# Kernel tuning notes

Measured on AMD Instinct MI355X. Metric: run time of the kernel, lower is better.

## Reference

```python
import jax, jax.numpy as jnp
import numpy as np

WINDOW_SIZE = 2
SOFTMAX_TEMP = 0.01


def get_indices(batch_size, window_size):
    # For each window, match keypoints of frame j against dense map of frame j+1.
    kp_inds, dense_inds = [], []
    for i in range(batch_size):
        for j in range(window_size - 1):
            idx = i * window_size + j
            kp_inds.append(idx)
            dense_inds.append(idx + 1)
    return np.array(kp_inds), np.array(dense_inds)


def l2_normalize(x, axis):
    n = jnp.sqrt(jnp.sum(x * x, axis=axis, keepdims=True))
    return x / jnp.maximum(n, 1e-12)


def grid_sample_bilinear(img, grid_u, grid_v):
    """torch.nn.functional.grid_sample, mode='bilinear', padding='zeros', align_corners=False.
    img: (B,C,H,W); grid_u, grid_v: (B,N) normalized coords in [-1,1]. Returns (B,C,N)."""
    B, C, H, W = img.shape
    x = ((grid_u + 1.0) * W - 1.0) * 0.5  # pixel x
    y = ((grid_v + 1.0) * H - 1.0) * 0.5  # pixel y
    x0 = jnp.floor(x)
    y0 = jnp.floor(y)
    wx1 = x - x0
    wy1 = y - y0
    flat = img.reshape(B, C, H * W)

    def gather(xi, yi):
        valid = (xi >= 0) & (xi <= W - 1) & (yi >= 0) & (yi <= H - 1)
        xi_c = jnp.clip(xi, 0, W - 1).astype(jnp.int32)
        yi_c = jnp.clip(yi, 0, H - 1).astype(jnp.int32)
        idx = yi_c * W + xi_c  # (B,N)
        vals = jnp.take_along_axis(flat, idx[:, None, :], axis=2)  # (B,C,N)
        return vals * valid[:, None, :].astype(img.dtype)

    out = (gather(x0, y0) * ((1 - wx1) * (1 - wy1))[:, None, :]
           + gather(x0 + 1, y0) * (wx1 * (1 - wy1))[:, None, :]
           + gather(x0, y0 + 1) * ((1 - wx1) * wy1)[:, None, :]
           + gather(x0 + 1, y0 + 1) * (wx1 * wy1)[:, None, :])
    return out


def setup_inputs() -> dict:
    key = jax.random.key(0)
    k1, k2, k3, k4 = jax.random.split(key, 4)
    BW, C, N, H, W = 8, 128, 512, 256, 256
    return {
        "keypoint_scores": jax.random.uniform(k1, (BW, 1, N), dtype=jnp.float32),
        "keypoint_desc": jax.random.normal(k2, (BW, C, N), dtype=jnp.float32),
        "scores_dense": jax.random.uniform(k3, (BW, 1, H, W), dtype=jnp.float32),
        "desc_dense": jax.random.normal(k4, (BW, C, H, W), dtype=jnp.float32),
    }


def reference(keypoint_scores, keypoint_desc, scores_dense, desc_dense):
    BW, C, N = keypoint_desc.shape
    batch_size = BW // WINDOW_SIZE
    _, _, H, W = desc_dense.shape
    kp_inds, dense_inds = get_indices(batch_size, WINDOW_SIZE)

    src_desc = l2_normalize(keypoint_desc[kp_inds], axis=1)  # (B,C,N)
    B = src_desc.shape[0]
    tgt_desc_dense = desc_dense[dense_inds]  # (B,C,H,W)
    tgt_unrolled = l2_normalize(tgt_desc_dense.reshape(B, C, H * W), axis=1)

    # cosine similarity scores (B,N,H*W) -> temperature softmax over dense map
    match_vals = jnp.einsum('bcn,bcm->bnm', src_desc, tgt_unrolled)
    soft_match_vals = jax.nn.softmax(match_vals / SOFTMAX_TEMP, axis=2)

    # soft-argmax: expected (u,v) pixel coordinates
    v_coord, u_coord = jnp.meshgrid(jnp.arange(H), jnp.arange(W), indexing='ij')
    coords = jnp.stack([u_coord.reshape(-1), v_coord.reshape(-1)], axis=1).astype(jnp.float32)  # (HW,2)
    pseudo_coords = jnp.einsum('bnm,mk->bnk', soft_match_vals, coords)  # (B,N,2)

    u_norm = 2.0 * pseudo_coords[:, :, 0] / (W - 1) - 1.0
    v_norm = 2.0 * pseudo_coords[:, :, 1] / (H - 1) - 1.0

    tgt_scores_dense = scores_dense[dense_inds]
    pseudo_scores = grid_sample_bilinear(tgt_scores_dense, u_norm, v_norm)  # (B,1,N)
    pseudo_desc = grid_sample_bilinear(tgt_desc_dense, u_norm, v_norm)      # (B,C,N)

    desc_match_score = jnp.sum(src_desc * pseudo_desc, axis=1, keepdims=True) / float(C)
    src_scores = keypoint_scores[kp_inds]
    match_weights = 0.5 * (desc_match_score + 1.0) * src_scores * pseudo_scores
    return (pseudo_coords, match_weights, soft_match_vals)
```

## Files before the change

kernel.cpp:

```cpp
#include <hip/hip_runtime.h>


typedef short  v8s __attribute__((ext_vector_type(8)));
typedef unsigned short v8u __attribute__((ext_vector_type(8)));
typedef float  v4f __attribute__((ext_vector_type(4)));

#define EXP2_SCALE 144.269504088896f
#define WAITV(N) asm volatile("s_waitcnt vmcnt(" #N ")" ::: "memory")
#define SBAR()   __builtin_amdgcn_s_barrier()
#define SCHED()  __builtin_amdgcn_sched_barrier(0)

static const size_t O_AHI  = 0;
static const size_t O_ALO  = O_AHI  + 262144ull*2;
static const size_t O_SRCN = O_ALO  + 262144ull*2;
static const size_t O_BHI  = O_SRCN + 262144ull*4;
static const size_t O_BLO  = O_BHI  + 33554432ull*2;
static const size_t O_PART = O_BLO  + 33554432ull*2;
static const size_t O_ROWS = O_PART + 2048ull*512*16;

static __device__ inline unsigned short f2bf(float x) {
    unsigned u = __float_as_uint(x);
    u = u + 0x7FFFu + ((u >> 16) & 1u);
    return (unsigned short)(u >> 16);
}
static __device__ inline float bf2f(unsigned short h) {
    return __uint_as_float(((unsigned)h) << 16);
}

__device__ __forceinline__ void gl_lds16(const void* g, void* l) {
    auto gp = (const __attribute__((address_space(1))) unsigned int*)(uintptr_t)g;
    auto lp = (__attribute__((address_space(3))) unsigned int*)(uintptr_t)l;
    __builtin_amdgcn_global_load_lds(gp, lp, 16, 0, 0);
}

__global__ void __launch_bounds__(256) k_prep_src(const float* __restrict__ kd,
                                                  float* __restrict__ srcN,
                                                  unsigned short* __restrict__ Ahi,
                                                  unsigned short* __restrict__ Alo) {
    int gw = blockIdx.x * 4 + (threadIdx.x >> 6);
    int l  = threadIdx.x & 63;
    int b  = gw >> 9, n = gw & 511;
    const float* base = kd + (size_t)(2 * b) * 128 * 512;
    float x0 = base[l * 512 + n];
    float x1 = base[(l + 64) * 512 + n];
    float ss = x0 * x0 + x1 * x1;
#pragma unroll
    for (int m = 1; m < 64; m <<= 1) ss += __shfl_xor(ss, m, 64);
    float inv = 1.0f / fmaxf(sqrtf(ss), 1e-12f);
    float xn0 = x0 * inv, xn1 = x1 * inv;
    int ob = gw * 128;
    srcN[ob + l] = xn0;  srcN[ob + l + 64] = xn1;
    unsigned short h0 = f2bf(xn0), h1 = f2bf(xn1);
    Ahi[ob + l] = h0;        Ahi[ob + l + 64] = h1;
    Alo[ob + l] = f2bf(xn0 - bf2f(h0));
    Alo[ob + l + 64] = f2bf(xn1 - bf2f(h1));
}

__global__ void __launch_bounds__(256) k_prep_tgt(const float* __restrict__ dd,
                                                  unsigned short* __restrict__ Bhi,
                                                  unsigned short* __restrict__ Blo) {
    int t = blockIdx.x * 128 + (threadIdx.x >> 1);
    int h = threadIdx.x & 1;
    int b = t >> 16;
    int p = t & 65535;
    const float* src = dd + (size_t)(2 * b + 1) * 128 * 65536 + (size_t)(h * 64) * 65536 + p;
    float v[64];
    float ss = 0.f;
#pragma unroll
    for (int c = 0; c < 64; ++c) { float x = src[(size_t)c * 65536]; v[c] = x; ss += x * x; }
    ss += __shfl_xor(ss, 1, 64);
    float inv = 1.0f / fmaxf(sqrtf(ss), 1e-12f);
    size_t ob = (size_t)t * 128 + h * 64;
#pragma unroll
    for (int c8 = 0; c8 < 8; ++c8) {
        v8u h8, l8;
#pragma unroll
        for (int j = 0; j < 8; ++j) {
            float xn = v[c8 * 8 + j] * inv;
            unsigned short hh = f2bf(xn);
            h8[j] = hh;
            l8[j] = f2bf(xn - bf2f(hh));
        }
        *(v8u*)(Bhi + ob + c8 * 8) = h8;
        *(v8u*)(Blo + ob + c8 * 8) = l8;
    }
}

template <int MODE>
__global__ void __launch_bounds__(512, 2) k_gemm(const unsigned short* __restrict__ Ahi,
                                                 const unsigned short* __restrict__ Alo,
                                                 const unsigned short* __restrict__ Bhi,
                                                 const unsigned short* __restrict__ Blo,
                                                 const float4* __restrict__ rows,
                                                 float* __restrict__ part,
                                                 float* __restrict__ out,
                                                 const float* __restrict__ ksc,
                                                 const float* __restrict__ sd,
                                                 const float* __restrict__ dd,
                                                 const float* __restrict__ srcN) {
    __shared__ v4f bstage4[4096];
    char* bstage = (char*)bstage4;

    const int tid = threadIdx.x;
    const int l = tid & 63, w = tid >> 6;
    const int wm = w >> 2, wn = w & 3;
    const int l15 = l & 15, l16 = l >> 4;
    const int mtg = blockIdx.x, ny = blockIdx.y, b = blockIdx.z;
    const int mt0 = mtg * 16;
    float* osm = out + 6144;

    v8s ahi[2][4], alo[2][4];
    {
        const size_t ar = ((size_t)(b * 512 + ny * 128 + wn * 32 + l15)) * 128 + l16 * 8;
#pragma unroll
        for (int nf = 0; nf < 2; ++nf)
#pragma unroll
            for (int ksl = 0; ksl < 4; ++ksl) {
                ahi[nf][ksl] = *(const v8s*)(Ahi + ar + nf * 2048 + ksl * 32);
                alo[nf][ksl] = *(const v8s*)(Alo + ar + nf * 2048 + ksl * 32);
            }
    }
    float invs[2];
    if (MODE == 1) {
#pragma unroll
        for (int nf = 0; nf < 2; ++nf)
            invs[nf] = rows[b * 512 + ny * 128 + wn * 32 + nf * 16 + l15].x;
    }
    WAITV(0);

    size_t pxrow = ((size_t)b * 65536 + (size_t)mt0 * 128) * 128;

#define STAGEU(SRC, prow, bufidx)                                                   \
    {                                                                               \
        const unsigned short* src_ = (SRC) + (prow);                                \
        char* dst_ = bstage + (bufidx) * 32768;                                     \
        _Pragma("unroll")                                                           \
        for (int i = 0; i < 4; ++i) {                                               \
            int sl = tid + i * 512;                                                 \
            int rl = sl >> 4, gg = sl & 15;                                         \
            gl_lds16(src_ + rl * 128 + ((gg ^ (rl & 15)) << 3), dst_ + (sl << 4));  \
        }                                                                           \
    }

#define PXF(bufbase, mf_, ksl_)                                                     \
    (*(const v8s*)((bufbase) + (wm * 64 + (mf_) * 16 + l15) * 256 +                 \
                   ((((ksl_) * 4 + l16) ^ ((wm * 64 + (mf_) * 16 + l15) & 15)) << 4)))

    v4f acc[4][2];

    if (MODE == 0) {
        STAGEU(Bhi, pxrow, 0);
        for (int mt = 0; mt < 16; ++mt) {
            if (mt < 15) STAGEU(Bhi, pxrow + 16384, (mt + 1) & 1);
            if (mt == 0) WAITV(4); else if (mt == 15) WAITV(0); else WAITV(6);
            SBAR(); SCHED();
            const char* bb = bstage + (mt & 1) * 32768;
#pragma unroll
            for (int mf = 0; mf < 4; ++mf)
#pragma unroll
                for (int nf = 0; nf < 2; ++nf) { v4f z = {0.f,0.f,0.f,0.f}; acc[mf][nf] = z; }
#pragma unroll
            for (int ksl = 0; ksl < 4; ++ksl) {
                v8s pxf[4];
#pragma unroll
                for (int mf = 0; mf < 4; ++mf) pxf[mf] = PXF(bb, mf, ksl);
#pragma unroll
                for (int mf = 0; mf < 4; ++mf)
#pragma unroll
                    for (int nf = 0; nf < 2; ++nf) {
                        acc[mf][nf] = __builtin_amdgcn_mfma_f32_16x16x32_bf16(pxf[mf], ahi[nf][ksl], acc[mf][nf], 0, 0, 0);
                        acc[mf][nf] = __builtin_amdgcn_mfma_f32_16x16x32_bf16(pxf[mf], alo[nf][ksl], acc[mf][nf], 0, 0, 0);
                    }
            }
            SCHED(); SBAR();
            float sS[2] = {0.f, 0.f}, sM[2] = {0.f, 0.f};
#pragma unroll
            for (int mf = 0; mf < 4; ++mf) {
                int mloc = wm * 64 + mf * 16 + l16 * 4;
#pragma unroll
                for (int nf = 0; nf < 2; ++nf)
#pragma unroll
                    for (int r = 0; r < 4; ++r) {
                        float e = __builtin_amdgcn_exp2f(fmaf(acc[mf][nf][r], EXP2_SCALE, -EXP2_SCALE));
                        sS[nf] += e;
                        sM[nf] = fmaf(e, (float)(mloc + r), sM[nf]);
                    }
            }
#pragma unroll
            for (int nf = 0; nf < 2; ++nf) {
                sS[nf] += __shfl_xor(sS[nf], 16, 64); sS[nf] += __shfl_xor(sS[nf], 32, 64);
                sM[nf] += __shfl_xor(sM[nf], 16, 64); sM[nf] += __shfl_xor(sM[nf], 32, 64);
            }
            if (l < 16) {
#pragma unroll
                for (int nf = 0; nf < 2; ++nf) {
                    int row = b * 512 + ny * 128 + wn * 32 + nf * 16 + l15;
                    *(float2*)(part + (((size_t)row * 512 + (mt0 + mt)) * 2 + wm) * 2)
                        = make_float2(sS[nf], sM[nf]);
                }
            }
            pxrow += 16384;
        }
    } else {
        STAGEU(Bhi, pxrow, 0);
        for (int mt = 0; mt < 16; ++mt) {
            STAGEU(Blo, pxrow, 1);
            if (mt == 0) WAITV(4); else WAITV(12);
            SBAR(); SCHED();
            const char* b0 = bstage;
#pragma unroll
            for (int mf = 0; mf < 4; ++mf)
#pragma unroll
                for (int nf = 0; nf < 2; ++nf) { v4f z = {0.f,0.f,0.f,0.f}; acc[mf][nf] = z; }
#pragma unroll
            for (int ksl = 0; ksl < 4; ++ksl) {
                v8s pxf[4];
#pragma unroll
                for (int mf = 0; mf < 4; ++mf) pxf[mf] = PXF(b0, mf, ksl);
#pragma unroll
                for (int mf = 0; mf < 4; ++mf)
#pragma unroll
                    for (int nf = 0; nf < 2; ++nf) {
                        acc[mf][nf] = __builtin_amdgcn_mfma_f32_16x16x32_bf16(pxf[mf], ahi[nf][ksl], acc[mf][nf], 0, 0, 0);
                        acc[mf][nf] = __builtin_amdgcn_mfma_f32_16x16x32_bf16(pxf[mf], alo[nf][ksl], acc[mf][nf], 0, 0, 0);
                    }
            }
            SCHED(); SBAR();
            if (mt < 15) STAGEU(Bhi, pxrow + 16384, 0);
            if (mt == 15) WAITV(0); else WAITV(4);
            SBAR(); SCHED();
            const char* b1 = bstage + 32768;
#pragma unroll
            for (int ksl = 0; ksl < 4; ++ksl) {
                v8s pxf[4];
#pragma unroll
                for (int mf = 0; mf < 4; ++mf) pxf[mf] = PXF(b1, mf, ksl);
#pragma unroll
                for (int mf = 0; mf < 4; ++mf)
#pragma unroll
                    for (int nf = 0; nf < 2; ++nf)
                        acc[mf][nf] = __builtin_amdgcn_mfma_f32_16x16x32_bf16(pxf[mf], ahi[nf][ksl], acc[mf][nf], 0, 0, 0);
            }
            SCHED(); SBAR();
            size_t mg0 = (size_t)(mt0 + mt) * 128 + wm * 64 + l16 * 4;
#pragma unroll
            for (int mf = 0; mf < 4; ++mf)
#pragma unroll
                for (int nf = 0; nf < 2; ++nf) {
                    v4f pv;
#pragma unroll
                    for (int r = 0; r < 4; ++r)
                        pv[r] = __builtin_amdgcn_exp2f(fmaf(acc[mf][nf][r], EXP2_SCALE, -EXP2_SCALE)) * invs[nf];
                    size_t ng = (size_t)(b * 512 + ny * 128 + wn * 32 + nf * 16 + l15);
                    __builtin_nontemporal_store(pv, (v4f*)(osm + ng * 65536 + mg0 + mf * 16));
                }
            pxrow += 16384;
        }

        if (w < 4) {
            const int bidx = mtg + 32 * ny + 128 * b;
            const int r = bidx * 4 + w;
            const int rb = r >> 9;
            float4 rs = rows[r];
            float u = rs.y, v = rs.z;
            float un = 2.0f * u / 255.0f - 1.0f;
            float vn = 2.0f * v / 255.0f - 1.0f;
            float x = ((un + 1.0f) * 256.0f - 1.0f) * 0.5f;
            float y = ((vn + 1.0f) * 256.0f - 1.0f) * 0.5f;
            float x0f = floorf(x), y0f = floorf(y);
            int x0 = (int)x0f, y0 = (int)y0f;
            int x1 = x0 + 1, y1 = y0 + 1;
            float wx1 = x - x0f, wy1 = y - y0f;
            float wx0 = 1.0f - wx1, wy0 = 1.0f - wy1;
            float m00 = ((x0 >= 0) & (x0 <= 255) & (y0 >= 0) & (y0 <= 255)) ? 1.f : 0.f;
            float m10 = ((x1 >= 0) & (x1 <= 255) & (y0 >= 0) & (y0 <= 255)) ? 1.f : 0.f;
            float m01 = ((x0 >= 0) & (x0 <= 255) & (y1 >= 0) & (y1 <= 255)) ? 1.f : 0.f;
            float m11 = ((x1 >= 0) & (x1 <= 255) & (y1 >= 0) & (y1 <= 255)) ? 1.f : 0.f;
            int cx0 = min(max(x0, 0), 255), cx1 = min(max(x1, 0), 255);
            int cy0 = min(max(y0, 0), 255), cy1 = min(max(y1, 0), 255);
            int i00 = cy0 * 256 + cx0, i10 = cy0 * 256 + cx1;
            int i01 = cy1 * 256 + cx0, i11 = cy1 * 256 + cx1;
            float w00 = wx0 * wy0 * m00, w10 = wx1 * wy0 * m10;
            float w01 = wx0 * wy1 * m01, w11 = wx1 * wy1 * m11;

            const float* sdb = sd + (size_t)(2 * rb + 1) * 65536;
            float ps = w00 * sdb[i00] + w10 * sdb[i10] + w01 * sdb[i01] + w11 * sdb[i11];

            const float* ddb = dd + (size_t)(2 * rb + 1) * 128 * 65536;
            float dot = 0.f;
#pragma unroll
            for (int h2 = 0; h2 < 2; ++h2) {
                int c = l + h2 * 64;
                const float* dc = ddb + (size_t)c * 65536;
                float pd = w00 * dc[i00] + w10 * dc[i10] + w01 * dc[i01] + w11 * dc[i11];
                dot += srcN[r * 128 + c] * pd;
            }
#pragma unroll
            for (int m = 1; m < 64; m <<= 1) dot += __shfl_xor(dot, m, 64);
            if (l == 0) {
                float dms = dot / 128.0f;
                float sscore = ksc[(2 * rb) * 512 + (r & 511)];
                out[4096 + r] = 0.5f * (dms + 1.0f) * sscore * ps;
            }
        }
    }
#undef STAGEU
#undef PXF
}

__global__ void __launch_bounds__(256) k_reduce(const float4* __restrict__ part,
                                                float4* __restrict__ rows,
                                                float* __restrict__ out) {
    int r = blockIdx.x * 4 + (threadIdx.x >> 6);
    int l = threadIdx.x & 63;
    float S = 0.f, Su = 0.f, Sv = 0.f;
#pragma unroll
    for (int i = 0; i < 8; ++i) {
        int mt = l + i * 64;
        float4 pp = part[(size_t)r * 512 + mt];
        float Sp = pp.x + pp.z;
        float Mp = pp.y + pp.w;
        S += Sp;
        Su += (float)((mt & 1) * 128) * Sp + Mp;
        Sv += (float)(mt >> 1) * Sp;
    }
#pragma unroll
    for (int m = 1; m < 64; m <<= 1) {
        S += __shfl_xor(S, m, 64);
        Su += __shfl_xor(Su, m, 64);
        Sv += __shfl_xor(Sv, m, 64);
    }
    if (l == 0) {
        float invS = 1.0f / S;
        float u = Su * invS, v = Sv * invS;
        rows[r] = make_float4(invS, u, v, 0.f);
        out[r * 2] = u;
        out[r * 2 + 1] = v;
    }
}

extern "C" void kernel_launch(void* const* d_in, const int* in_sizes, int n_in,
                              void* d_out, int out_size, void* d_ws, size_t ws_size,
                              hipStream_t stream) {
    const float* ksc = (const float*)d_in[0];
    const float* kd  = (const float*)d_in[1];
    const float* sd  = (const float*)d_in[2];
    const float* dd  = (const float*)d_in[3];
    float* out = (float*)d_out;
    char* ws = (char*)d_ws;

    unsigned short* Ahi  = (unsigned short*)(ws + O_AHI);
    unsigned short* Alo  = (unsigned short*)(ws + O_ALO);
    float*          srcN = (float*)(ws + O_SRCN);
    unsigned short* Bhi  = (unsigned short*)(ws + O_BHI);
    unsigned short* Blo  = (unsigned short*)(ws + O_BLO);
    float*          part = (float*)(ws + O_PART);
    float4*         rows = (float4*)(ws + O_ROWS);

    k_prep_src<<<512, 256, 0, stream>>>(kd, srcN, Ahi, Alo);
    k_prep_tgt<<<2048, 256, 0, stream>>>(dd, Bhi, Blo);
    k_gemm<0><<<dim3(32, 4, 4), 512, 0, stream>>>(Ahi, Alo, Bhi, Blo, rows, part, out, ksc, sd, dd, srcN);
    k_reduce<<<512, 256, 0, stream>>>((const float4*)part, rows, out);
    k_gemm<1><<<dim3(32, 4, 4), 512, 0, stream>>>(Ahi, Alo, Bhi, Blo, rows, part, out, ksc, sd, dd, srcN);
}
```

Baseline: 411.6 us.

## Fuse all five kernels into one persistent kernel with grid barriers

Replaces the five separate launches (prep_src, prep_tgt, two GEMM passes, reduce) with a single 256-block persistent kernel. The phases are separated by software grid barriers built on an atomic counter, and a memset resets the counter before launch. Each block now handles two GEMM tiles per pass and a slice of the prep and reduce work. This removes launch gaps and per-kernel tail effects, at the cost of spin-wait barrier overhead. It also relies on all 256 blocks being co-resident, and it drops the __launch_bounds__(512,2) occupancy hint.

```diff
diff --git a/kernel.cpp b/kernel.cpp
--- a/kernel.cpp
+++ b/kernel.cpp
@@ -17,6 +17,7 @@
 static const size_t O_BLO  = O_BHI  + 33554432ull*2;
 static const size_t O_PART = O_BLO  + 33554432ull*2;
 static const size_t O_ROWS = O_PART + 2048ull*512*16;
+static const size_t O_BAR  = O_ROWS + 2048ull*16;
 
 static __device__ inline unsigned short f2bf(float x) {
     unsigned u = __float_as_uint(x);
@@ -33,71 +34,30 @@
     __builtin_amdgcn_global_load_lds(gp, lp, 16, 0, 0);
 }
 
-__global__ void __launch_bounds__(256) k_prep_src(const float* __restrict__ kd,
-                                                  float* __restrict__ srcN,
-                                                  unsigned short* __restrict__ Ahi,
-                                                  unsigned short* __restrict__ Alo) {
-    int gw = blockIdx.x * 4 + (threadIdx.x >> 6);
-    int l  = threadIdx.x & 63;
-    int b  = gw >> 9, n = gw & 511;
-    const float* base = kd + (size_t)(2 * b) * 128 * 512;
-    float x0 = base[l * 512 + n];
-    float x1 = base[(l + 64) * 512 + n];
-    float ss = x0 * x0 + x1 * x1;
-#pragma unroll
-    for (int m = 1; m < 64; m <<= 1) ss += __shfl_xor(ss, m, 64);
-    float inv = 1.0f / fmaxf(sqrtf(ss), 1e-12f);
-    float xn0 = x0 * inv, xn1 = x1 * inv;
-    int ob = gw * 128;
-    srcN[ob + l] = xn0;  srcN[ob + l + 64] = xn1;
-    unsigned short h0 = f2bf(xn0), h1 = f2bf(xn1);
-    Ahi[ob + l] = h0;        Ahi[ob + l + 64] = h1;
-    Alo[ob + l] = f2bf(xn0 - bf2f(h0));
-    Alo[ob + l + 64] = f2bf(xn1 - bf2f(h1));
-}
-
-__global__ void __launch_bounds__(256) k_prep_tgt(const float* __restrict__ dd,
-                                                  unsigned short* __restrict__ Bhi,
-                                                  unsigned short* __restrict__ Blo) {
-    int t = blockIdx.x * 128 + (threadIdx.x >> 1);
-    int h = threadIdx.x & 1;
-    int b = t >> 16;
-    int p = t & 65535;
-    const float* src = dd + (size_t)(2 * b + 1) * 128 * 65536 + (size_t)(h * 64) * 65536 + p;
-    float v[64];
-    float ss = 0.f;
-#pragma unroll
-    for (int c = 0; c < 64; ++c) { float x = src[(size_t)c * 65536]; v[c] = x; ss += x * x; }
-    ss += __shfl_xor(ss, 1, 64);
-    float inv = 1.0f / fmaxf(sqrtf(ss), 1e-12f);
-    size_t ob = (size_t)t * 128 + h * 64;
-#pragma unroll
-    for (int c8 = 0; c8 < 8; ++c8) {
-        v8u h8, l8;
-#pragma unroll
-        for (int j = 0; j < 8; ++j) {
-            float xn = v[c8 * 8 + j] * inv;
-            unsigned short hh = f2bf(xn);
-            h8[j] = hh;
-            l8[j] = f2bf(xn - bf2f(hh));
-        }
-        *(v8u*)(Bhi + ob + c8 * 8) = h8;
-        *(v8u*)(Blo + ob + c8 * 8) = l8;
-    }
-}
-
-template <int MODE>
-__global__ void __launch_bounds__(512, 2) k_gemm(const unsigned short* __restrict__ Ahi,
-                                                 const unsigned short* __restrict__ Alo,
-                                                 const unsigned short* __restrict__ Bhi,
-                                                 const unsigned short* __restrict__ Blo,
-                                                 const float4* __restrict__ rows,
-                                                 float* __restrict__ part,
-                                                 float* __restrict__ out,
-                                                 const float* __restrict__ ksc,
-                                                 const float* __restrict__ sd,
-                                                 const float* __restrict__ dd,
-                                                 const float* __restrict__ srcN) {
+__device__ __forceinline__ void gbar(unsigned* ctr) {
+    __syncthreads();
+    if (threadIdx.x == 0) {
+        __threadfence();
+        atomicAdd(ctr, 1u);
+        while (atomicAdd(ctr, 0u) < 256u) __builtin_amdgcn_s_sleep(2);
+        __threadfence();
+    }
+    __syncthreads();
+}
+
+__global__ void __launch_bounds__(512) k_mega(const float* __restrict__ ksc,
+                                              const float* __restrict__ kd,
+                                              const float* __restrict__ sd,
+                                              const float* __restrict__ dd,
+                                              float* __restrict__ out,
+                                              unsigned short* __restrict__ Ahi,
+                                              unsigned short* __restrict__ Alo,
+                                              float* __restrict__ srcN,
+                                              unsigned short* __restrict__ Bhi,
+                                              unsigned short* __restrict__ Blo,
+                                              float* __restrict__ part,
+                                              float4* __restrict__ rows,
+                                              unsigned* __restrict__ bar) {
     __shared__ v4f bstage4[4096];
     char* bstage = (char*)bstage4;
 
@@ -105,30 +65,56 @@
     const int l = tid & 63, w = tid >> 6;
     const int wm = w >> 2, wn = w & 3;
     const int l15 = l & 15, l16 = l >> 4;
-    const int mtg = blockIdx.x, ny = blockIdx.y, b = blockIdx.z;
-    const int mt0 = mtg * 16;
     float* osm = out + 6144;
 
-    v8s ahi[2][4], alo[2][4];
     {
-        const size_t ar = ((size_t)(b * 512 + ny * 128 + wn * 32 + l15)) * 128 + l16 * 8;
-#pragma unroll
-        for (int nf = 0; nf < 2; ++nf)
-#pragma unroll
-            for (int ksl = 0; ksl < 4; ++ksl) {
-                ahi[nf][ksl] = *(const v8s*)(Ahi + ar + nf * 2048 + ksl * 32);
-                alo[nf][ksl] = *(const v8s*)(Alo + ar + nf * 2048 + ksl * 32);
-            }
-    }
-    float invs[2];
-    if (MODE == 1) {
-#pragma unroll
-        for (int nf = 0; nf < 2; ++nf)
-            invs[nf] = rows[b * 512 + ny * 128 + wn * 32 + nf * 16 + l15].x;
-    }
-    WAITV(0);
-
-    size_t pxrow = ((size_t)b * 65536 + (size_t)mt0 * 128) * 128;
+        int gw = blockIdx.x * 8 + w;
+        int b = gw >> 9, n = gw & 511;
+        const float* base = kd + (size_t)(2 * b) * 128 * 512;
+        float x0 = base[l * 512 + n];
+        float x1 = base[(l + 64) * 512 + n];
+        float ss = x0 * x0 + x1 * x1;
+#pragma unroll
+        for (int m = 1; m < 64; m <<= 1) ss += __shfl_xor(ss, m, 64);
+        float inv = 1.0f / fmaxf(sqrtf(ss), 1e-12f);
+        float xn0 = x0 * inv, xn1 = x1 * inv;
+        int ob = gw * 128;
+        srcN[ob + l] = xn0;  srcN[ob + l + 64] = xn1;
+        unsigned short h0 = f2bf(xn0), h1 = f2bf(xn1);
+        Ahi[ob + l] = h0;        Ahi[ob + l + 64] = h1;
+        Alo[ob + l] = f2bf(xn0 - bf2f(h0));
+        Alo[ob + l + 64] = f2bf(xn1 - bf2f(h1));
+    }
+    {
+        int h = tid & 1;
+#pragma unroll 1
+        for (int it = 0; it < 4; ++it) {
+            int t = blockIdx.x * 1024 + it * 256 + (tid >> 1);
+            int b = t >> 16, p = t & 65535;
+            const float* src = dd + (size_t)(2 * b + 1) * 128 * 65536 + (size_t)(h * 64) * 65536 + p;
+            float v[64];
+            float ss = 0.f;
+#pragma unroll
+            for (int c = 0; c < 64; ++c) { float x = src[(size_t)c * 65536]; v[c] = x; ss += x * x; }
+            ss += __shfl_xor(ss, 1, 64);
+            float inv = 1.0f / fmaxf(sqrtf(ss), 1e-12f);
+            size_t ob = (size_t)t * 128 + h * 64;
+#pragma unroll
+            for (int c8 = 0; c8 < 8; ++c8) {
+                v8u h8, l8;
+#pragma unroll
+                for (int j = 0; j < 8; ++j) {
+                    float xn = v[c8 * 8 + j] * inv;
+                    unsigned short hh = f2bf(xn);
+                    h8[j] = hh;
+                    l8[j] = f2bf(xn - bf2f(hh));
+                }
+                *(v8u*)(Bhi + ob + c8 * 8) = h8;
+                *(v8u*)(Blo + ob + c8 * 8) = l8;
+            }
+        }
+    }
+    gbar(bar + 0);
 
 #define STAGEU(SRC, prow, bufidx)                                                   \
     {                                                                               \
@@ -141,15 +127,34 @@
             gl_lds16(src_ + rl * 128 + ((gg ^ (rl & 15)) << 3), dst_ + (sl << 4));  \
         }                                                                           \
     }
-
 #define PXF(bufbase, mf_, ksl_)                                                     \
     (*(const v8s*)((bufbase) + (wm * 64 + (mf_) * 16 + l15) * 256 +                 \
                    ((((ksl_) * 4 + l16) ^ ((wm * 64 + (mf_) * 16 + l15) & 15)) << 4)))
 
     v4f acc[4][2];
 
-    if (MODE == 0) {
+#pragma unroll 1
+    for (int u = 0; u < 2; ++u) {
+        const int id = blockIdx.x * 2 + u;
+        const int b = id >> 7, ny = (id >> 5) & 3, mtg = id & 31;
+        const int mt0 = mtg * 16;
+
+        v8s ahi[2][4], alo[2][4];
+        {
+            const size_t ar = ((size_t)(b * 512 + ny * 128 + wn * 32 + l15)) * 128 + l16 * 8;
+#pragma unroll
+            for (int nf = 0; nf < 2; ++nf)
+#pragma unroll
+                for (int ksl = 0; ksl < 4; ++ksl) {
+                    ahi[nf][ksl] = *(const v8s*)(Ahi + ar + nf * 2048 + ksl * 32);
+                    alo[nf][ksl] = *(const v8s*)(Alo + ar + nf * 2048 + ksl * 32);
+                }
+        }
+        WAITV(0);
+
+        size_t pxrow = ((size_t)b * 65536 + (size_t)mt0 * 128) * 128;
         STAGEU(Bhi, pxrow, 0);
+#pragma unroll 1
         for (int mt = 0; mt < 16; ++mt) {
             if (mt < 15) STAGEU(Bhi, pxrow + 16384, (mt + 1) & 1);
             if (mt == 0) WAITV(4); else if (mt == 15) WAITV(0); else WAITV(6);
@@ -201,8 +206,64 @@
             }
             pxrow += 16384;
         }
-    } else {
+    }
+    gbar(bar + 1);
+
+    {
+        int r = blockIdx.x * 8 + w;
+        const float4* p4 = (const float4*)part;
+        float S = 0.f, Su = 0.f, Sv = 0.f;
+#pragma unroll
+        for (int i = 0; i < 8; ++i) {
+            int mt = l + i * 64;
+            float4 pp = p4[(size_t)r * 512 + mt];
+            float Sp = pp.x + pp.z, Mp = pp.y + pp.w;
+            S += Sp;
+            Su += (float)((mt & 1) * 128) * Sp + Mp;
+            Sv += (float)(mt >> 1) * Sp;
+        }
+#pragma unroll
+        for (int m = 1; m < 64; m <<= 1) {
+            S += __shfl_xor(S, m, 64);
+            Su += __shfl_xor(Su, m, 64);
+            Sv += __shfl_xor(Sv, m, 64);
+        }
+        if (l == 0) {
+            float invS = 1.0f / S;
+            float uu = Su * invS, vv = Sv * invS;
+            rows[r] = make_float4(invS, uu, vv, 0.f);
+            out[r * 2] = uu;
+            out[r * 2 + 1] = vv;
+        }
+    }
+    gbar(bar + 2);
+
+#pragma unroll 1
+    for (int u = 0; u < 2; ++u) {
+        const int id = blockIdx.x * 2 + u;
+        const int b = id >> 7, ny = (id >> 5) & 3, mtg = id & 31;
+        const int mt0 = mtg * 16;
+
+        v8s ahi[2][4], alo[2][4];
+        {
+            const size_t ar = ((size_t)(b * 512 + ny * 128 + wn * 32 + l15)) * 128 + l16 * 8;
+#pragma unroll
+            for (int nf = 0; nf < 2; ++nf)
+#pragma unroll
+                for (int ksl = 0; ksl < 4; ++ksl) {
+                    ahi[nf][ksl] = *(const v8s*)(Ahi + ar + nf * 2048 + ksl * 32);
+                    alo[nf][ksl] = *(const v8s*)(Alo + ar + nf * 2048 + ksl * 32);
+                }
+        }
+        float invs[2];
+#pragma unroll
+        for (int nf = 0; nf < 2; ++nf)
+            invs[nf] = rows[b * 512 + ny * 128 + wn * 32 + nf * 16 + l15].x;
+        WAITV(0);
+
+        size_t pxrow = ((size_t)b * 65536 + (size_t)mt0 * 128) * 128;
         STAGEU(Bhi, pxrow, 0);
+#pragma unroll 1
         for (int mt = 0; mt < 16; ++mt) {
             STAGEU(Blo, pxrow, 1);
             if (mt == 0) WAITV(4); else WAITV(12);
@@ -256,86 +317,54 @@
                 }
             pxrow += 16384;
         }
-
-        if (w < 4) {
-            const int bidx = mtg + 32 * ny + 128 * b;
-            const int r = bidx * 4 + w;
-            const int rb = r >> 9;
-            float4 rs = rows[r];
-            float u = rs.y, v = rs.z;
-            float un = 2.0f * u / 255.0f - 1.0f;
-            float vn = 2.0f * v / 255.0f - 1.0f;
-            float x = ((un + 1.0f) * 256.0f - 1.0f) * 0.5f;
-            float y = ((vn + 1.0f) * 256.0f - 1.0f) * 0.5f;
-            float x0f = floorf(x), y0f = floorf(y);
-            int x0 = (int)x0f, y0 = (int)y0f;
-            int x1 = x0 + 1, y1 = y0 + 1;
-            float wx1 = x - x0f, wy1 = y - y0f;
-            float wx0 = 1.0f - wx1, wy0 = 1.0f - wy1;
-            float m00 = ((x0 >= 0) & (x0 <= 255) & (y0 >= 0) & (y0 <= 255)) ? 1.f : 0.f;
-            float m10 = ((x1 >= 0) & (x1 <= 255) & (y0 >= 0) & (y0 <= 255)) ? 1.f : 0.f;
-            float m01 = ((x0 >= 0) & (x0 <= 255) & (y1 >= 0) & (y1 <= 255)) ? 1.f : 0.f;
-            float m11 = ((x1 >= 0) & (x1 <= 255) & (y1 >= 0) & (y1 <= 255)) ? 1.f : 0.f;
-            int cx0 = min(max(x0, 0), 255), cx1 = min(max(x1, 0), 255);
-            int cy0 = min(max(y0, 0), 255), cy1 = min(max(y1, 0), 255);
-            int i00 = cy0 * 256 + cx0, i10 = cy0 * 256 + cx1;
-            int i01 = cy1 * 256 + cx0, i11 = cy1 * 256 + cx1;
-            float w00 = wx0 * wy0 * m00, w10 = wx1 * wy0 * m10;
-            float w01 = wx0 * wy1 * m01, w11 = wx1 * wy1 * m11;
-
-            const float* sdb = sd + (size_t)(2 * rb + 1) * 65536;
-            float ps = w00 * sdb[i00] + w10 * sdb[i10] + w01 * sdb[i01] + w11 * sdb[i11];
-
-            const float* ddb = dd + (size_t)(2 * rb + 1) * 128 * 65536;
-            float dot = 0.f;
-#pragma unroll
-            for (int h2 = 0; h2 < 2; ++h2) {
-                int c = l + h2 * 64;
-                const float* dc = ddb + (size_t)c * 65536;
-                float pd = w00 * dc[i00] + w10 * dc[i10] + w01 * dc[i01] + w11 * dc[i11];
-                dot += srcN[r * 128 + c] * pd;
-            }
-#pragma unroll
-            for (int m = 1; m < 64; m <<= 1) dot += __shfl_xor(dot, m, 64);
-            if (l == 0) {
-                float dms = dot / 128.0f;
-                float sscore = ksc[(2 * rb) * 512 + (r & 511)];
-                out[4096 + r] = 0.5f * (dms + 1.0f) * sscore * ps;
-            }
-        }
     }
 #undef STAGEU
 #undef PXF
-}
-
-__global__ void __launch_bounds__(256) k_reduce(const float4* __restrict__ part,
-                                                float4* __restrict__ rows,
-                                                float* __restrict__ out) {
-    int r = blockIdx.x * 4 + (threadIdx.x >> 6);
-    int l = threadIdx.x & 63;
-    float S = 0.f, Su = 0.f, Sv = 0.f;
-#pragma unroll
-    for (int i = 0; i < 8; ++i) {
-        int mt = l + i * 64;
-        float4 pp = part[(size_t)r * 512 + mt];
-        float Sp = pp.x + pp.z;
-        float Mp = pp.y + pp.w;
-        S += Sp;
-        Su += (float)((mt & 1) * 128) * Sp + Mp;
-        Sv += (float)(mt >> 1) * Sp;
-    }
-#pragma unroll
-    for (int m = 1; m < 64; m <<= 1) {
-        S += __shfl_xor(S, m, 64);
-        Su += __shfl_xor(Su, m, 64);
-        Sv += __shfl_xor(Sv, m, 64);
-    }
-    if (l == 0) {
-        float invS = 1.0f / S;
-        float u = Su * invS, v = Sv * invS;
-        rows[r] = make_float4(invS, u, v, 0.f);
-        out[r * 2] = u;
-        out[r * 2 + 1] = v;
+
+    {
+        const int r = blockIdx.x * 8 + w;
+        const int rb = r >> 9;
+        float4 rs = rows[r];
+        float u = rs.y, v = rs.z;
+        float un = 2.0f * u / 255.0f - 1.0f;
+        float vn = 2.0f * v / 255.0f - 1.0f;
+        float x = ((un + 1.0f) * 256.0f - 1.0f) * 0.5f;
+        float y = ((vn + 1.0f) * 256.0f - 1.0f) * 0.5f;
+        float x0f = floorf(x), y0f = floorf(y);
+        int x0 = (int)x0f, y0 = (int)y0f;
+        int x1 = x0 + 1, y1 = y0 + 1;
+        float wx1 = x - x0f, wy1 = y - y0f;
+        float wx0 = 1.0f - wx1, wy0 = 1.0f - wy1;
+        float m00 = ((x0 >= 0) & (x0 <= 255) & (y0 >= 0) & (y0 <= 255)) ? 1.f : 0.f;
+        float m10 = ((x1 >= 0) & (x1 <= 255) & (y0 >= 0) & (y0 <= 255)) ? 1.f : 0.f;
+        float m01 = ((x0 >= 0) & (x0 <= 255) & (y1 >= 0) & (y1 <= 255)) ? 1.f : 0.f;
+        float m11 = ((x1 >= 0) & (x1 <= 255) & (y1 >= 0) & (y1 <= 255)) ? 1.f : 0.f;
+        int cx0 = min(max(x0, 0), 255), cx1 = min(max(x1, 0), 255);
+        int cy0 = min(max(y0, 0), 255), cy1 = min(max(y1, 0), 255);
+        int i00 = cy0 * 256 + cx0, i10 = cy0 * 256 + cx1;
+        int i01 = cy1 * 256 + cx0, i11 = cy1 * 256 + cx1;
+        float w00 = wx0 * wy0 * m00, w10 = wx1 * wy0 * m10;
+        float w01 = wx0 * wy1 * m01, w11 = wx1 * wy1 * m11;
+
+        const float* sdb = sd + (size_t)(2 * rb + 1) * 65536;
+        float ps = w00 * sdb[i00] + w10 * sdb[i10] + w01 * sdb[i01] + w11 * sdb[i11];
+
+        const float* ddb = dd + (size_t)(2 * rb + 1) * 128 * 65536;
+        float dot = 0.f;
+#pragma unroll
+        for (int h2 = 0; h2 < 2; ++h2) {
+            int c = l + h2 * 64;
+            const float* dc = ddb + (size_t)c * 65536;
+            float pd = w00 * dc[i00] + w10 * dc[i10] + w01 * dc[i01] + w11 * dc[i11];
+            dot += srcN[r * 128 + c] * pd;
+        }
+#pragma unroll
+        for (int m = 1; m < 64; m <<= 1) dot += __shfl_xor(dot, m, 64);
+        if (l == 0) {
+            float dms = dot / 128.0f;
+            float sscore = ksc[(2 * rb) * 512 + (r & 511)];
+            out[4096 + r] = 0.5f * (dms + 1.0f) * sscore * ps;
+        }
     }
 }
 
@@ -356,10 +385,9 @@
     unsigned short* Blo  = (unsigned short*)(ws + O_BLO);
     float*          part = (float*)(ws + O_PART);
     float4*         rows = (float4*)(ws + O_ROWS);
-
-    k_prep_src<<<512, 256, 0, stream>>>(kd, srcN, Ahi, Alo);
-    k_prep_tgt<<<2048, 256, 0, stream>>>(dd, Bhi, Blo);
-    k_gemm<0><<<dim3(32, 4, 4), 512, 0, stream>>>(Ahi, Alo, Bhi, Blo, rows, part, out, ksc, sd, dd, srcN);
-    k_reduce<<<512, 256, 0, stream>>>((const float4*)part, rows, out);
-    k_gemm<1><<<dim3(32, 4, 4), 512, 0, stream>>>(Ahi, Alo, Bhi, Blo, rows, part, out, ksc, sd, dd, srcN);
-}
+    unsigned*       bar  = (unsigned*)(ws + O_BAR);
+
+    hipMemsetAsync(bar, 0, 64, stream);
+    k_mega<<<256, 512, 0, stream>>>(ksc, kd, sd, dd, out, Ahi, Alo, srcN,
+                                    Bhi, Blo, part, rows, bar);
+}
```

Result: slower. 482.3 us (+17.2%).

## Triple-buffer LDS staging of dense descriptor tiles in both GEMM passes

Applied to the files above, without the earlier changes.

Grows the shared-memory staging area from two to three 32KB buffers and prefetches two tiles ahead in both kernel modes. In mode 1 the hi and lo tile loads become a single 32-phase ring, so each load overlaps the previous phase's MFMA work instead of waiting behind it. Barriers are moved so the exp/store epilogue runs before the next barrier. The goal is to hide global-load latency better, at the cost of more LDS per block, which could reduce occupancy at two blocks per CU.

```diff
diff --git a/kernel.cpp b/kernel.cpp
--- a/kernel.cpp
+++ b/kernel.cpp
@@ -98,7 +98,7 @@
                                                  const float* __restrict__ sd,
                                                  const float* __restrict__ dd,
                                                  const float* __restrict__ srcN) {
-    __shared__ v4f bstage4[4096];
+    __shared__ v4f bstage4[6144];
     char* bstage = (char*)bstage4;
 
     const int tid = threadIdx.x;
@@ -128,7 +128,7 @@
     }
     WAITV(0);
 
-    size_t pxrow = ((size_t)b * 65536 + (size_t)mt0 * 128) * 128;
+    const size_t pxbase = ((size_t)b * 65536 + (size_t)mt0 * 128) * 128;
 
 #define STAGEU(SRC, prow, bufidx)                                                   \
     {                                                                               \
@@ -141,7 +141,6 @@
             gl_lds16(src_ + rl * 128 + ((gg ^ (rl & 15)) << 3), dst_ + (sl << 4));  \
         }                                                                           \
     }
-
 #define PXF(bufbase, mf_, ksl_)                                                     \
     (*(const v8s*)((bufbase) + (wm * 64 + (mf_) * 16 + l15) * 256 +                 \
                    ((((ksl_) * 4 + l16) ^ ((wm * 64 + (mf_) * 16 + l15) & 15)) << 4)))
@@ -149,12 +148,18 @@
     v4f acc[4][2];
 
     if (MODE == 0) {
-        STAGEU(Bhi, pxrow, 0);
+        STAGEU(Bhi, pxbase, 0);
+        STAGEU(Bhi, pxbase + 16384, 1);
+#pragma unroll 1
         for (int mt = 0; mt < 16; ++mt) {
-            if (mt < 15) STAGEU(Bhi, pxrow + 16384, (mt + 1) & 1);
-            if (mt == 0) WAITV(4); else if (mt == 15) WAITV(0); else WAITV(6);
+            if (mt < 14) STAGEU(Bhi, pxbase + (size_t)(mt + 2) * 16384, (mt + 2) % 3);
+            if (mt == 0) WAITV(8);
+            else if (mt == 1) WAITV(10);
+            else if (mt == 14) WAITV(8);
+            else if (mt == 15) WAITV(4);
+            else WAITV(12);
             SBAR(); SCHED();
-            const char* bb = bstage + (mt & 1) * 32768;
+            const char* bb = bstage + (mt % 3) * 32768;
 #pragma unroll
             for (int mf = 0; mf < 4; ++mf)
 #pragma unroll
@@ -172,7 +177,7 @@
                         acc[mf][nf] = __builtin_amdgcn_mfma_f32_16x16x32_bf16(pxf[mf], alo[nf][ksl], acc[mf][nf], 0, 0, 0);
                     }
             }
-            SCHED(); SBAR();
+            SCHED();
             float sS[2] = {0.f, 0.f}, sM[2] = {0.f, 0.f};
 #pragma unroll
             for (int mf = 0; mf < 4; ++mf) {
@@ -199,62 +204,71 @@
                         = make_float2(sS[nf], sM[nf]);
                 }
             }
-            pxrow += 16384;
+            SBAR();
         }
     } else {
-        STAGEU(Bhi, pxrow, 0);
-        for (int mt = 0; mt < 16; ++mt) {
-            STAGEU(Blo, pxrow, 1);
-            if (mt == 0) WAITV(4); else WAITV(12);
+        STAGEU(Bhi, pxbase, 0);
+        STAGEU(Blo, pxbase, 1);
+#pragma unroll 1
+        for (int ph = 0; ph < 32; ++ph) {
+            if (ph < 30) {
+                size_t prow2 = pxbase + (size_t)((ph + 2) >> 1) * 16384;
+                if ((ph & 1) == 0) STAGEU(Bhi, prow2, (ph + 2) % 3)
+                else               STAGEU(Blo, prow2, (ph + 2) % 3)
+            }
+            if (ph <= 1) WAITV(8);
+            else if (ph == 30) WAITV(12);
+            else if (ph == 31) WAITV(8);
+            else WAITV(16);
             SBAR(); SCHED();
-            const char* b0 = bstage;
-#pragma unroll
-            for (int mf = 0; mf < 4; ++mf)
-#pragma unroll
-                for (int nf = 0; nf < 2; ++nf) { v4f z = {0.f,0.f,0.f,0.f}; acc[mf][nf] = z; }
-#pragma unroll
-            for (int ksl = 0; ksl < 4; ++ksl) {
-                v8s pxf[4];
-#pragma unroll
-                for (int mf = 0; mf < 4; ++mf) pxf[mf] = PXF(b0, mf, ksl);
+            const char* bb = bstage + (ph % 3) * 32768;
+            if ((ph & 1) == 0) {
 #pragma unroll
                 for (int mf = 0; mf < 4; ++mf)
 #pragma unroll
+                    for (int nf = 0; nf < 2; ++nf) { v4f z = {0.f,0.f,0.f,0.f}; acc[mf][nf] = z; }
+#pragma unroll
+                for (int ksl = 0; ksl < 4; ++ksl) {
+                    v8s pxf[4];
+#pragma unroll
+                    for (int mf = 0; mf < 4; ++mf) pxf[mf] = PXF(bb, mf, ksl);
+#pragma unroll
+                    for (int mf = 0; mf < 4; ++mf)
+#pragma unroll
+                        for (int nf = 0; nf < 2; ++nf) {
+                            acc[mf][nf] = __builtin_amdgcn_mfma_f32_16x16x32_bf16(pxf[mf], ahi[nf][ksl], acc[mf][nf], 0, 0, 0);
+                            acc[mf][nf] = __builtin_amdgcn_mfma_f32_16x16x32_bf16(pxf[mf], alo[nf][ksl], acc[mf][nf], 0, 0, 0);
+                        }
+                }
+                SCHED(); SBAR();
+            } else {
+#pragma unroll
+                for (int ksl = 0; ksl < 4; ++ksl) {
+                    v8s pxf[4];
+#pragma unroll
+                    for (int mf = 0; mf < 4; ++mf) pxf[mf] = PXF(bb, mf, ksl);
+#pragma unroll
+                    for (int mf = 0; mf < 4; ++mf)
+#pragma unroll
+                        for (int nf = 0; nf < 2; ++nf)
+                            acc[mf][nf] = __builtin_amdgcn_mfma_f32_16x16x32_bf16(pxf[mf], ahi[nf][ksl], acc[mf][nf], 0, 0, 0);
+                }
+                SCHED();
+                int mt = ph >> 1;
+                size_t mg0 = (size_t)(mt0 + mt) * 128 + wm * 64 + l16 * 4;
+#pragma unroll
+                for (int mf = 0; mf < 4; ++mf)
+#pragma unroll
                     for (int nf = 0; nf < 2; ++nf) {
-                        acc[mf][nf] = __builtin_amdgcn_mfma_f32_16x16x32_bf16(pxf[mf], ahi[nf][ksl], acc[mf][nf], 0, 0, 0);
-                        acc[mf][nf] = __builtin_amdgcn_mfma_f32_16x16x32_bf16(pxf[mf], alo[nf][ksl], acc[mf][nf], 0, 0, 0);
+                        v4f pv;
+#pragma unroll
+                        for (int r = 0; r < 4; ++r)
+                            pv[r] = __builtin_amdgcn_exp2f(fmaf(acc[mf][nf][r], EXP2_SCALE, -EXP2_SCALE)) * invs[nf];
+                        size_t ng = (size_t)(b * 512 + ny * 128 + wn * 32 + nf * 16 + l15);
+                        __builtin_nontemporal_store(pv, (v4f*)(osm + ng * 65536 + mg0 + mf * 16));
                     }
-            }
-            SCHED(); SBAR();
-            if (mt < 15) STAGEU(Bhi, pxrow + 16384, 0);
-            if (mt == 15) WAITV(0); else WAITV(4);
-            SBAR(); SCHED();
-            const char* b1 = bstage + 32768;
-#pragma unroll
-            for (int ksl = 0; ksl < 4; ++ksl) {
-                v8s pxf[4];
-#pragma unroll
-                for (int mf = 0; mf < 4; ++mf) pxf[mf] = PXF(b1, mf, ksl);
-#pragma unroll
-                for (int mf = 0; mf < 4; ++mf)
-#pragma unroll
-                    for (int nf = 0; nf < 2; ++nf)
-                        acc[mf][nf] = __builtin_amdgcn_mfma_f32_16x16x32_bf16(pxf[mf], ahi[nf][ksl], acc[mf][nf], 0, 0, 0);
-            }
-            SCHED(); SBAR();
-            size_t mg0 = (size_t)(mt0 + mt) * 128 + wm * 64 + l16 * 4;
-#pragma unroll
-            for (int mf = 0; mf < 4; ++mf)
-#pragma unroll
-                for (int nf = 0; nf < 2; ++nf) {
-                    v4f pv;
-#pragma unroll
-                    for (int r = 0; r < 4; ++r)
-                        pv[r] = __builtin_amdgcn_exp2f(fmaf(acc[mf][nf][r], EXP2_SCALE, -EXP2_SCALE)) * invs[nf];
-                    size_t ng = (size_t)(b * 512 + ny * 128 + wn * 32 + nf * 16 + l15);
-                    __builtin_nontemporal_store(pv, (v4f*)(osm + ng * 65536 + mg0 + mf * 16));
-                }
-            pxrow += 16384;
+                SBAR();
+            }
         }
 
         if (w < 4) {
```

Result: no change. 407.8 us (-0.9%).
